# Performance work log

Measured on AMD Instinct MI355X. Metric: run time of the kernel, lower is better.

## Reference

```python
import jax, jax.numpy as jnp
import numpy as np

EPS = 1e-6
B, H, V, DH = 4096, 16, 8, 128


def setup_inputs() -> dict:
    key = jax.random.key(0)
    ks = jax.random.split(key, 7)
    s = 1.0 / np.sqrt(DH)  # ~ torch Linear init scale
    return {
        "iso_heads": jax.random.normal(ks[0], (B, H, DH), jnp.float32),
        "view_head_tokens": jax.random.normal(ks[1], (B, H, V, DH), jnp.float32),
        "pi": jax.random.uniform(ks[2], (B, H, V), jnp.float32),
        "Wq": jax.random.normal(ks[3], (H, DH, DH), jnp.float32) * s,
        "Wk": jax.random.normal(ks[4], (H, DH, DH), jnp.float32) * s,
        "Wv": jax.random.normal(ks[5], (H, DH, DH), jnp.float32) * s,
        "Wo": jax.random.normal(ks[6], (H, DH, DH), jnp.float32) * s,
    }


def reference(iso_heads, view_head_tokens, pi, Wq, Wk, Wv, Wo):
    # Per-head linears: torch Linear(y = x @ W.T), W stored (out, in) -> 'hed' (e=out, d=in)
    q = jnp.einsum("bhd,hed->bhe", iso_heads, Wq)            # [B,H,Dh]
    k = jnp.einsum("bhvd,hed->bhve", view_head_tokens, Wk)   # [B,H,V,Dh]
    v = jnp.einsum("bhvd,hed->bhve", view_head_tokens, Wv)   # [B,H,V,Dh]
    # Single-query attention per head with additive log-prior bias
    scores = jnp.einsum("bhd,bhvd->bhv", q, k) / jnp.sqrt(jnp.float32(DH))
    scores = scores + jnp.log(pi + EPS)
    attn = jax.nn.softmax(scores, axis=-1)                   # dropout = identity (eval)
    ctx = jnp.einsum("bhv,bhvd->bhd", attn, v)               # [B,H,Dh]
    out = jnp.einsum("bhd,hed->bhe", ctx, Wo)                # [B,H,Dh]
    return (out, attn)
```

## Files before the change

kernel.cpp:

```cpp
#include <hip/hip_runtime.h>
#include <cstdint>
#include <cstddef>

#define H_  16
#define V_  8
#define DH_ 128
#define B_  4096
#define BT  32
#define LDST 132

__global__ __launch_bounds__(256) void precompute_MN(
    const float* __restrict__ Wq, const float* __restrict__ Wk,
    const float* __restrict__ Wv, const float* __restrict__ Wo,
    float* __restrict__ Mmat, float* __restrict__ NTmat)
{
    const int bx    = blockIdx.x;
    const int which = bx & 1;
    const int h     = (bx >> 1) & 15;
    const int chunk = bx >> 5;
    const int tid   = threadIdx.x;
    const int col   = tid & 127;
    const int r     = chunk * 2 + (tid >> 7);

    float acc = 0.f;
    if (which == 0) {
        const float* wq = Wq + h * DH_ * DH_;
        const float* wk = Wk + h * DH_ * DH_;
#pragma unroll 8
        for (int e = 0; e < DH_; ++e)
            acc += wq[e * DH_ + r] * wk[e * DH_ + col];
        Mmat[h * DH_ * DH_ + (size_t)r * DH_ + col] = acc;
    } else {
        const float* wo = Wo + h * DH_ * DH_;
        const float* wv = Wv + h * DH_ * DH_;
#pragma unroll 8
        for (int d = 0; d < DH_; ++d)
            acc += wo[(size_t)r * DH_ + d] * wv[d * DH_ + col];
        NTmat[h * DH_ * DH_ + (size_t)col * DH_ + r] = acc;
    }
}

__global__ __launch_bounds__(256, 3) void fused_attn(
    const float* __restrict__ iso, const float* __restrict__ view,
    const float* __restrict__ pi,
    const float* __restrict__ Mmat, const float* __restrict__ NTmat,
    float* __restrict__ out, float* __restrict__ attn_out)
{
    __shared__ float wbuf[64 * DH_];
    __shared__ float row_s[BT][LDST];
    __shared__ float at_s[BT][V_];

    const int tid = threadIdx.x;
    const int h   = blockIdx.x >> 7;
    const int b0  = (blockIdx.x & 127) * BT;

    const int tx = tid & 31;
    const int ty = tid >> 5;

    const float* Mh = Mmat  + (size_t)h * DH_ * DH_;
    const float* Nh = NTmat + (size_t)h * DH_ * DH_;

#pragma unroll
    for (int i = 0; i < 4; ++i) {
        const int idx = tid + i * 256;
        const int r   = idx >> 5;
        const int q   = idx & 31;
        *(float4*)&row_s[r][q * 4] =
            *(const float4*)(iso + ((size_t)(b0 + r) * H_ + h) * DH_ + q * 4);
    }
#pragma unroll
    for (int i = 0; i < 8; ++i) {
        const int idx = tid + i * 256;
        *(float4*)&wbuf[idx * 4] = *(const float4*)(Mh + (size_t)idx * 4);
    }
    __syncthreads();

    float acc[4][4];
#pragma unroll
    for (int i = 0; i < 4; ++i)
#pragma unroll
        for (int j = 0; j < 4; ++j) acc[i][j] = 0.f;

    auto mac64 = [&](int dbase) {
#pragma unroll 4
        for (int dd = 0; dd < 64; dd += 4) {
            const float4 m0 = *(const float4*)&wbuf[(dd + 0) * DH_ + tx * 4];
            const float4 m1 = *(const float4*)&wbuf[(dd + 1) * DH_ + tx * 4];
            const float4 m2 = *(const float4*)&wbuf[(dd + 2) * DH_ + tx * 4];
            const float4 m3 = *(const float4*)&wbuf[(dd + 3) * DH_ + tx * 4];
#pragma unroll
            for (int i = 0; i < 4; ++i) {
                const float4 a = *(const float4*)&row_s[ty * 4 + i][dbase + dd];
                acc[i][0] += a.x * m0.x + a.y * m1.x + a.z * m2.x + a.w * m3.x;
                acc[i][1] += a.x * m0.y + a.y * m1.y + a.z * m2.y + a.w * m3.y;
                acc[i][2] += a.x * m0.z + a.y * m1.z + a.z * m2.z + a.w * m3.z;
                acc[i][3] += a.x * m0.w + a.y * m1.w + a.z * m2.w + a.w * m3.w;
            }
        }
    };

    mac64(0);
    __syncthreads();

#pragma unroll
    for (int i = 0; i < 8; ++i) {
        const int idx = tid + i * 256;
        *(float4*)&wbuf[idx * 4] = *(const float4*)(Mh + 8192 + (size_t)idx * 4);
    }
    __syncthreads();

    mac64(64);

#pragma unroll
    for (int i = 0; i < 4; ++i)
        *(float4*)&row_s[ty * 4 + i][tx * 4] =
            make_float4(acc[i][0], acc[i][1], acc[i][2], acc[i][3]);

    {
        const int w    = tid >> 6;
        const int lane = tid & 63;
        const int g    = lane >> 3;
        const int i8   = lane & 7;

        for (int r = 0; r < 8; ++r) {
            const int row   = w * 8 + r;
            const size_t bh = (size_t)(b0 + row) * H_ + h;
            const float* vp = view + (bh * V_ + g) * DH_ + i8 * 16;
            const float* qp = &row_s[row][i8 * 16];
            const float4 x0 = *(const float4*)(vp + 0);
            const float4 x1 = *(const float4*)(vp + 4);
            const float4 x2 = *(const float4*)(vp + 8);
            const float4 x3 = *(const float4*)(vp + 12);
            const float4 q0 = *(const float4*)(qp + 0);
            const float4 q1 = *(const float4*)(qp + 4);
            const float4 q2 = *(const float4*)(qp + 8);
            const float4 q3 = *(const float4*)(qp + 12);
            float s = x0.x*q0.x + x0.y*q0.y + x0.z*q0.z + x0.w*q0.w
                    + x1.x*q1.x + x1.y*q1.y + x1.z*q1.z + x1.w*q1.w
                    + x2.x*q2.x + x2.y*q2.y + x2.z*q2.z + x2.w*q2.w
                    + x3.x*q3.x + x3.y*q3.y + x3.z*q3.z + x3.w*q3.w;
            s += __shfl_xor(s, 1);
            s += __shfl_xor(s, 2);
            s += __shfl_xor(s, 4);
            if (i8 == 0) {
                float sc = s * 0.08838834764831845f
                         + logf(pi[bh * V_ + g] + 1e-6f);
                float mx = sc;
                mx = fmaxf(mx, __shfl_xor(mx, 8));
                mx = fmaxf(mx, __shfl_xor(mx, 16));
                mx = fmaxf(mx, __shfl_xor(mx, 32));
                const float ex = expf(sc - mx);
                float den = ex;
                den += __shfl_xor(den, 8);
                den += __shfl_xor(den, 16);
                den += __shfl_xor(den, 32);
                const float at = ex / den;
                at_s[row][g] = at;
                attn_out[bh * V_ + g] = at;
            }
        }

        const int half = lane >> 5;
        const int c    = lane & 31;
#pragma unroll
        for (int t = 0; t < 4; ++t) {
            const int row   = w * 8 + t * 2 + half;
            const size_t bh = (size_t)(b0 + row) * H_ + h;
            const float* vb = view + bh * V_ * DH_ + c * 4;
            float4 cx = make_float4(0.f, 0.f, 0.f, 0.f);
#pragma unroll
            for (int v = 0; v < V_; ++v) {
                const float a  = at_s[row][v];
                const float4 x = *(const float4*)(vb + (size_t)v * DH_);
                cx.x += a * x.x; cx.y += a * x.y; cx.z += a * x.z; cx.w += a * x.w;
            }
            *(float4*)&row_s[row][c * 4] = cx;
        }
    }
    __syncthreads();

#pragma unroll
    for (int i = 0; i < 8; ++i) {
        const int idx = tid + i * 256;
        *(float4*)&wbuf[idx * 4] = *(const float4*)(Nh + (size_t)idx * 4);
    }
    __syncthreads();

#pragma unroll
    for (int i = 0; i < 4; ++i)
#pragma unroll
        for (int j = 0; j < 4; ++j) acc[i][j] = 0.f;

    mac64(0);
    __syncthreads();

#pragma unroll
    for (int i = 0; i < 8; ++i) {
        const int idx = tid + i * 256;
        *(float4*)&wbuf[idx * 4] = *(const float4*)(Nh + 8192 + (size_t)idx * 4);
    }
    __syncthreads();

    mac64(64);

#pragma unroll
    for (int i = 0; i < 4; ++i)
        *(float4*)(out + ((size_t)(b0 + ty * 4 + i) * H_ + h) * DH_ + tx * 4) =
            make_float4(acc[i][0], acc[i][1], acc[i][2], acc[i][3]);
}

extern "C" void kernel_launch(void* const* d_in, const int* in_sizes, int n_in,
                              void* d_out, int out_size, void* d_ws, size_t ws_size,
                              hipStream_t stream)
{
    const float* iso  = (const float*)d_in[0];
    const float* view = (const float*)d_in[1];
    const float* pi   = (const float*)d_in[2];
    const float* Wq   = (const float*)d_in[3];
    const float* Wk   = (const float*)d_in[4];
    const float* Wv   = (const float*)d_in[5];
    const float* Wo   = (const float*)d_in[6];

    float* out  = (float*)d_out;
    float* attn = out + (size_t)B_ * H_ * DH_;

    float* Mmat  = (float*)d_ws;
    float* NTmat = Mmat + (size_t)H_ * DH_ * DH_;

    hipLaunchKernelGGL(precompute_MN, dim3(2048), dim3(256), 0, stream,
                       Wq, Wk, Wv, Wo, Mmat, NTmat);
    hipLaunchKernelGGL(fused_attn, dim3(H_ * (B_ / BT)), dim3(256), 0, stream,
                       iso, view, pi, Mmat, NTmat, out, attn);
}
```

Measured before the change: 484.8 us.

## Use fp16 MFMA for per-head projections and restructure attention loop

Folded weight matrices are stored as fp16 and both per-head 32x128x128 projections run on MFMA 16x16x32 f16 instructions instead of scalar FMA, with the whole weight matrix staged in shared memory at once. The view-token loop now loads each row's tokens once and reuses them for both scores and context, prefetching the next row, and replaces log(pi) plus exp with pi times exp. The N weight load overlaps with the attention stage. This cuts ALU work and global re-reads of view, at the cost of fp16 rounding of activations and weights, and occupancy drops to 2 blocks per SM.

```diff
diff --git a/kernel.cpp b/kernel.cpp
--- a/kernel.cpp
+++ b/kernel.cpp
@@ -7,12 +7,18 @@
 #define DH_ 128
 #define B_  4096
 #define BT  32
-#define LDST 132
+
+#define LDW 136
+#define LDQ 132
+
+typedef _Float16 v8h __attribute__((ext_vector_type(8)));
+typedef _Float16 v4h __attribute__((ext_vector_type(4)));
+typedef float    v4f __attribute__((ext_vector_type(4)));
 
 __global__ __launch_bounds__(256) void precompute_MN(
     const float* __restrict__ Wq, const float* __restrict__ Wk,
     const float* __restrict__ Wv, const float* __restrict__ Wo,
-    float* __restrict__ Mmat, float* __restrict__ NTmat)
+    _Float16* __restrict__ MT16, _Float16* __restrict__ N216)
 {
     const int bx    = blockIdx.x;
     const int which = bx & 1;
@@ -28,185 +34,205 @@
         const float* wk = Wk + h * DH_ * DH_;
 #pragma unroll 8
         for (int e = 0; e < DH_; ++e)
-            acc += wq[e * DH_ + r] * wk[e * DH_ + col];
-        Mmat[h * DH_ * DH_ + (size_t)r * DH_ + col] = acc;
+            acc += wq[e * DH_ + col] * wk[e * DH_ + r];
+        MT16[(size_t)h * DH_ * DH_ + r * DH_ + col] = (_Float16)acc;
     } else {
         const float* wo = Wo + h * DH_ * DH_;
         const float* wv = Wv + h * DH_ * DH_;
 #pragma unroll 8
         for (int d = 0; d < DH_; ++d)
-            acc += wo[(size_t)r * DH_ + d] * wv[d * DH_ + col];
-        NTmat[h * DH_ * DH_ + (size_t)col * DH_ + r] = acc;
+            acc += wo[r * DH_ + d] * wv[d * DH_ + col];
+        N216[(size_t)h * DH_ * DH_ + r * DH_ + col] = (_Float16)acc;
     }
 }
 
-__global__ __launch_bounds__(256, 3) void fused_attn(
+__global__ __launch_bounds__(256, 2) void fused_attn(
     const float* __restrict__ iso, const float* __restrict__ view,
     const float* __restrict__ pi,
-    const float* __restrict__ Mmat, const float* __restrict__ NTmat,
+    const _Float16* __restrict__ MT16, const _Float16* __restrict__ N216,
     float* __restrict__ out, float* __restrict__ attn_out)
 {
-    __shared__ float wbuf[64 * DH_];
-    __shared__ float row_s[BT][LDST];
-    __shared__ float at_s[BT][V_];
+    __shared__ __align__(16) _Float16 w16[128 * LDW];
+    __shared__ __align__(16) _Float16 a16[BT * LDW];
+    __shared__ __align__(16) float    qk_s[BT * LDQ];
 
     const int tid = threadIdx.x;
     const int h   = blockIdx.x >> 7;
     const int b0  = (blockIdx.x & 127) * BT;
 
-    const int tx = tid & 31;
-    const int ty = tid >> 5;
-
-    const float* Mh = Mmat  + (size_t)h * DH_ * DH_;
-    const float* Nh = NTmat + (size_t)h * DH_ * DH_;
+    const int w    = tid >> 6;
+    const int lane = tid & 63;
+    const int rt   = w >> 1;
+    const int cb   = (w & 1) * 64;
+    const int fr   = lane & 15;
+    const int kg   = lane >> 4;
 
 #pragma unroll
     for (int i = 0; i < 4; ++i) {
         const int idx = tid + i * 256;
-        const int r   = idx >> 5;
-        const int q   = idx & 31;
-        *(float4*)&row_s[r][q * 4] =
-            *(const float4*)(iso + ((size_t)(b0 + r) * H_ + h) * DH_ + q * 4);
-    }
-#pragma unroll
-    for (int i = 0; i < 8; ++i) {
-        const int idx = tid + i * 256;
-        *(float4*)&wbuf[idx * 4] = *(const float4*)(Mh + (size_t)idx * 4);
+        const int r   = idx >> 5, c4 = idx & 31;
+        const float4 t = *(const float4*)(iso + ((size_t)(b0 + r) * H_ + h) * DH_ + c4 * 4);
+        v4h ht; ht[0] = (_Float16)t.x; ht[1] = (_Float16)t.y;
+                ht[2] = (_Float16)t.z; ht[3] = (_Float16)t.w;
+        *(v4h*)&a16[r * LDW + c4 * 4] = ht;
+    }
+    {
+        const _Float16* src = MT16 + (size_t)h * DH_ * DH_;
+#pragma unroll
+        for (int i = 0; i < 8; ++i) {
+            const int idx = tid + i * 256;
+            *(v8h*)&w16[(idx >> 4) * LDW + (idx & 15) * 8] = *(const v8h*)(src + idx * 8);
+        }
     }
     __syncthreads();
 
-    float acc[4][4];
-#pragma unroll
-    for (int i = 0; i < 4; ++i)
-#pragma unroll
-        for (int j = 0; j < 4; ++j) acc[i][j] = 0.f;
-
-    auto mac64 = [&](int dbase) {
-#pragma unroll 4
-        for (int dd = 0; dd < 64; dd += 4) {
-            const float4 m0 = *(const float4*)&wbuf[(dd + 0) * DH_ + tx * 4];
-            const float4 m1 = *(const float4*)&wbuf[(dd + 1) * DH_ + tx * 4];
-            const float4 m2 = *(const float4*)&wbuf[(dd + 2) * DH_ + tx * 4];
-            const float4 m3 = *(const float4*)&wbuf[(dd + 3) * DH_ + tx * 4];
-#pragma unroll
-            for (int i = 0; i < 4; ++i) {
-                const float4 a = *(const float4*)&row_s[ty * 4 + i][dbase + dd];
-                acc[i][0] += a.x * m0.x + a.y * m1.x + a.z * m2.x + a.w * m3.x;
-                acc[i][1] += a.x * m0.y + a.y * m1.y + a.z * m2.y + a.w * m3.y;
-                acc[i][2] += a.x * m0.z + a.y * m1.z + a.z * m2.z + a.w * m3.z;
-                acc[i][3] += a.x * m0.w + a.y * m1.w + a.z * m2.w + a.w * m3.w;
-            }
-        }
-    };
-
-    mac64(0);
+    {
+        v4f ac0 = {0,0,0,0}, ac1 = {0,0,0,0}, ac2 = {0,0,0,0}, ac3 = {0,0,0,0};
+#pragma unroll
+        for (int kt = 0; kt < 4; ++kt) {
+            const int ko = kt * 32 + kg * 8;
+            const v8h a  = *(const v8h*)&a16[(rt * 16 + fr) * LDW + ko];
+            const v8h bf0 = *(const v8h*)&w16[(cb +  0 + fr) * LDW + ko];
+            const v8h bf1 = *(const v8h*)&w16[(cb + 16 + fr) * LDW + ko];
+            const v8h bf2 = *(const v8h*)&w16[(cb + 32 + fr) * LDW + ko];
+            const v8h bf3 = *(const v8h*)&w16[(cb + 48 + fr) * LDW + ko];
+            ac0 = __builtin_amdgcn_mfma_f32_16x16x32_f16(a, bf0, ac0, 0, 0, 0);
+            ac1 = __builtin_amdgcn_mfma_f32_16x16x32_f16(a, bf1, ac1, 0, 0, 0);
+            ac2 = __builtin_amdgcn_mfma_f32_16x16x32_f16(a, bf2, ac2, 0, 0, 0);
+            ac3 = __builtin_amdgcn_mfma_f32_16x16x32_f16(a, bf3, ac3, 0, 0, 0);
+        }
+#pragma unroll
+        for (int g = 0; g < 4; ++g) {
+            const int row = rt * 16 + kg * 4 + g;
+            qk_s[row * LDQ + cb +  0 + fr] = ac0[g];
+            qk_s[row * LDQ + cb + 16 + fr] = ac1[g];
+            qk_s[row * LDQ + cb + 32 + fr] = ac2[g];
+            qk_s[row * LDQ + cb + 48 + fr] = ac3[g];
+        }
+    }
     __syncthreads();
 
-#pragma unroll
-    for (int i = 0; i < 8; ++i) {
-        const int idx = tid + i * 256;
-        *(float4*)&wbuf[idx * 4] = *(const float4*)(Mh + 8192 + (size_t)idx * 4);
-    }
-    __syncthreads();
-
-    mac64(64);
-
-#pragma unroll
-    for (int i = 0; i < 4; ++i)
-        *(float4*)&row_s[ty * 4 + i][tx * 4] =
-            make_float4(acc[i][0], acc[i][1], acc[i][2], acc[i][3]);
-
-    {
-        const int w    = tid >> 6;
-        const int lane = tid & 63;
-        const int g    = lane >> 3;
-        const int i8   = lane & 7;
-
+    {
+        const _Float16* src = N216 + (size_t)h * DH_ * DH_;
+#pragma unroll
+        for (int i = 0; i < 8; ++i) {
+            const int idx = tid + i * 256;
+            *(v8h*)&w16[(idx >> 4) * LDW + (idx & 15) * 8] = *(const v8h*)(src + idx * 8);
+        }
+    }
+
+    {
+        const int hl  = lane >> 5;
+        const int l32 = lane & 31;
+        const float SC = 0.08838834764831845f;
+
+        const float* vb = view + ((size_t)(b0 + w * 8) * H_ + h) * (V_ * DH_);
+        float4 x0 = *(const float4*)(vb +   0 + lane * 4);
+        float4 x1 = *(const float4*)(vb + 256 + lane * 4);
+        float4 x2 = *(const float4*)(vb + 512 + lane * 4);
+        float4 x3 = *(const float4*)(vb + 768 + lane * 4);
+
+#pragma unroll
         for (int r = 0; r < 8; ++r) {
             const int row   = w * 8 + r;
             const size_t bh = (size_t)(b0 + row) * H_ + h;
-            const float* vp = view + (bh * V_ + g) * DH_ + i8 * 16;
-            const float* qp = &row_s[row][i8 * 16];
-            const float4 x0 = *(const float4*)(vp + 0);
-            const float4 x1 = *(const float4*)(vp + 4);
-            const float4 x2 = *(const float4*)(vp + 8);
-            const float4 x3 = *(const float4*)(vp + 12);
-            const float4 q0 = *(const float4*)(qp + 0);
-            const float4 q1 = *(const float4*)(qp + 4);
-            const float4 q2 = *(const float4*)(qp + 8);
-            const float4 q3 = *(const float4*)(qp + 12);
-            float s = x0.x*q0.x + x0.y*q0.y + x0.z*q0.z + x0.w*q0.w
-                    + x1.x*q1.x + x1.y*q1.y + x1.z*q1.z + x1.w*q1.w
-                    + x2.x*q2.x + x2.y*q2.y + x2.z*q2.z + x2.w*q2.w
-                    + x3.x*q3.x + x3.y*q3.y + x3.z*q3.z + x3.w*q3.w;
-            s += __shfl_xor(s, 1);
-            s += __shfl_xor(s, 2);
-            s += __shfl_xor(s, 4);
-            if (i8 == 0) {
-                float sc = s * 0.08838834764831845f
-                         + logf(pi[bh * V_ + g] + 1e-6f);
-                float mx = sc;
-                mx = fmaxf(mx, __shfl_xor(mx, 8));
-                mx = fmaxf(mx, __shfl_xor(mx, 16));
-                mx = fmaxf(mx, __shfl_xor(mx, 32));
-                const float ex = expf(sc - mx);
-                float den = ex;
-                den += __shfl_xor(den, 8);
-                den += __shfl_xor(den, 16);
-                den += __shfl_xor(den, 32);
-                const float at = ex / den;
-                at_s[row][g] = at;
-                attn_out[bh * V_ + g] = at;
+
+            const v4f q4 = *(const v4f*)&qk_s[row * LDQ + l32 * 4];
+            float p0 = x0.x*q4[0] + x0.y*q4[1] + x0.z*q4[2] + x0.w*q4[3];
+            float p1 = x1.x*q4[0] + x1.y*q4[1] + x1.z*q4[2] + x1.w*q4[3];
+            float p2 = x2.x*q4[0] + x2.y*q4[1] + x2.z*q4[2] + x2.w*q4[3];
+            float p3 = x3.x*q4[0] + x3.y*q4[1] + x3.z*q4[2] + x3.w*q4[3];
+
+            float4 y0, y1, y2, y3;
+            if (r < 7) {
+                const float* vn = vb + H_ * V_ * DH_;
+                y0 = *(const float4*)(vn +   0 + lane * 4);
+                y1 = *(const float4*)(vn + 256 + lane * 4);
+                y2 = *(const float4*)(vn + 512 + lane * 4);
+                y3 = *(const float4*)(vn + 768 + lane * 4);
             }
-        }
-
-        const int half = lane >> 5;
-        const int c    = lane & 31;
-#pragma unroll
-        for (int t = 0; t < 4; ++t) {
-            const int row   = w * 8 + t * 2 + half;
-            const size_t bh = (size_t)(b0 + row) * H_ + h;
-            const float* vb = view + bh * V_ * DH_ + c * 4;
-            float4 cx = make_float4(0.f, 0.f, 0.f, 0.f);
-#pragma unroll
-            for (int v = 0; v < V_; ++v) {
-                const float a  = at_s[row][v];
-                const float4 x = *(const float4*)(vb + (size_t)v * DH_);
-                cx.x += a * x.x; cx.y += a * x.y; cx.z += a * x.z; cx.w += a * x.w;
+
+            p0 += __shfl_xor(p0, 1); p0 += __shfl_xor(p0, 2); p0 += __shfl_xor(p0, 4);
+            p0 += __shfl_xor(p0, 8); p0 += __shfl_xor(p0, 16);
+            p1 += __shfl_xor(p1, 1); p1 += __shfl_xor(p1, 2); p1 += __shfl_xor(p1, 4);
+            p1 += __shfl_xor(p1, 8); p1 += __shfl_xor(p1, 16);
+            p2 += __shfl_xor(p2, 1); p2 += __shfl_xor(p2, 2); p2 += __shfl_xor(p2, 4);
+            p2 += __shfl_xor(p2, 8); p2 += __shfl_xor(p2, 16);
+            p3 += __shfl_xor(p3, 1); p3 += __shfl_xor(p3, 2); p3 += __shfl_xor(p3, 4);
+            p3 += __shfl_xor(p3, 8); p3 += __shfl_xor(p3, 16);
+            const float o0 = __shfl_xor(p0, 32);
+            const float o1 = __shfl_xor(p1, 32);
+            const float o2 = __shfl_xor(p2, 32);
+            const float o3 = __shfl_xor(p3, 32);
+
+            const float4 pa = *(const float4*)(pi + bh * V_);
+            const float4 pb = *(const float4*)(pi + bh * V_ + 4);
+            const float pe0 = hl ? pa.y : pa.x,  po0 = hl ? pa.x : pa.y;
+            const float pe1 = hl ? pa.w : pa.z,  po1 = hl ? pa.z : pa.w;
+            const float pe2 = hl ? pb.y : pb.x,  po2 = hl ? pb.x : pb.y;
+            const float pe3 = hl ? pb.w : pb.z,  po3 = hl ? pb.z : pb.w;
+
+            const float s0 = p0 * SC, s1 = p1 * SC, s2 = p2 * SC, s3 = p3 * SC;
+            const float t0 = o0 * SC, t1 = o1 * SC, t2 = o2 * SC, t3 = o3 * SC;
+            const float m  = fmaxf(fmaxf(fmaxf(s0, s1), fmaxf(s2, s3)),
+                                   fmaxf(fmaxf(t0, t1), fmaxf(t2, t3)));
+            const float e0 = (pe0 + 1e-6f) * __expf(s0 - m);
+            const float e1 = (pe1 + 1e-6f) * __expf(s1 - m);
+            const float e2 = (pe2 + 1e-6f) * __expf(s2 - m);
+            const float e3 = (pe3 + 1e-6f) * __expf(s3 - m);
+            const float f0 = (po0 + 1e-6f) * __expf(t0 - m);
+            const float f1 = (po1 + 1e-6f) * __expf(t1 - m);
+            const float f2 = (po2 + 1e-6f) * __expf(t2 - m);
+            const float f3 = (po3 + 1e-6f) * __expf(t3 - m);
+            const float inv = 1.0f / (((e0 + e1) + (e2 + e3)) + ((f0 + f1) + (f2 + f3)));
+            const float a0 = e0 * inv, a1 = e1 * inv, a2 = e2 * inv, a3 = e3 * inv;
+
+            float cx = a0 * x0.x + a1 * x1.x + a2 * x2.x + a3 * x3.x;
+            float cy = a0 * x0.y + a1 * x1.y + a2 * x2.y + a3 * x3.y;
+            float cz = a0 * x0.z + a1 * x1.z + a2 * x2.z + a3 * x3.z;
+            float cw = a0 * x0.w + a1 * x1.w + a2 * x2.w + a3 * x3.w;
+            cx += __shfl_xor(cx, 32);
+            cy += __shfl_xor(cy, 32);
+            cz += __shfl_xor(cz, 32);
+            cw += __shfl_xor(cw, 32);
+            if (lane < 32) {
+                v4h ch; ch[0] = (_Float16)cx; ch[1] = (_Float16)cy;
+                        ch[2] = (_Float16)cz; ch[3] = (_Float16)cw;
+                *(v4h*)&a16[row * LDW + l32 * 4] = ch;
             }
-            *(float4*)&row_s[row][c * 4] = cx;
+            if (l32 == 0) {
+                float* ao = attn_out + bh * V_;
+                ao[0 + hl] = a0; ao[2 + hl] = a1; ao[4 + hl] = a2; ao[6 + hl] = a3;
+            }
+            if (r < 7) { vb += H_ * V_ * DH_; x0 = y0; x1 = y1; x2 = y2; x3 = y3; }
         }
     }
     __syncthreads();
 
-#pragma unroll
-    for (int i = 0; i < 8; ++i) {
-        const int idx = tid + i * 256;
-        *(float4*)&wbuf[idx * 4] = *(const float4*)(Nh + (size_t)idx * 4);
-    }
-    __syncthreads();
-
-#pragma unroll
-    for (int i = 0; i < 4; ++i)
-#pragma unroll
-        for (int j = 0; j < 4; ++j) acc[i][j] = 0.f;
-
-    mac64(0);
-    __syncthreads();
-
-#pragma unroll
-    for (int i = 0; i < 8; ++i) {
-        const int idx = tid + i * 256;
-        *(float4*)&wbuf[idx * 4] = *(const float4*)(Nh + 8192 + (size_t)idx * 4);
-    }
-    __syncthreads();
-
-    mac64(64);
-
-#pragma unroll
-    for (int i = 0; i < 4; ++i)
-        *(float4*)(out + ((size_t)(b0 + ty * 4 + i) * H_ + h) * DH_ + tx * 4) =
-            make_float4(acc[i][0], acc[i][1], acc[i][2], acc[i][3]);
+    {
+        v4f ac0 = {0,0,0,0}, ac1 = {0,0,0,0}, ac2 = {0,0,0,0}, ac3 = {0,0,0,0};
+#pragma unroll
+        for (int kt = 0; kt < 4; ++kt) {
+            const int ko = kt * 32 + kg * 8;
+            const v8h a  = *(const v8h*)&a16[(rt * 16 + fr) * LDW + ko];
+            const v8h bf0 = *(const v8h*)&w16[(cb +  0 + fr) * LDW + ko];
+            const v8h bf1 = *(const v8h*)&w16[(cb + 16 + fr) * LDW + ko];
+            const v8h bf2 = *(const v8h*)&w16[(cb + 32 + fr) * LDW + ko];
+            const v8h bf3 = *(const v8h*)&w16[(cb + 48 + fr) * LDW + ko];
+            ac0 = __builtin_amdgcn_mfma_f32_16x16x32_f16(a, bf0, ac0, 0, 0, 0);
+            ac1 = __builtin_amdgcn_mfma_f32_16x16x32_f16(a, bf1, ac1, 0, 0, 0);
+            ac2 = __builtin_amdgcn_mfma_f32_16x16x32_f16(a, bf2, ac2, 0, 0, 0);
+            ac3 = __builtin_amdgcn_mfma_f32_16x16x32_f16(a, bf3, ac3, 0, 0, 0);
+        }
+#pragma unroll
+        for (int g = 0; g < 4; ++g) {
+            float* op = out + (size_t)(b0 + rt * 16 + kg * 4 + g) * (H_ * DH_) + h * DH_;
+            op[cb +  0 + fr] = ac0[g];
+            op[cb + 16 + fr] = ac1[g];
+            op[cb + 32 + fr] = ac2[g];
+            op[cb + 48 + fr] = ac3[g];
+        }
+    }
 }
 
 extern "C" void kernel_launch(void* const* d_in, const int* in_sizes, int n_in,
@@ -224,11 +250,11 @@
     float* out  = (float*)d_out;
     float* attn = out + (size_t)B_ * H_ * DH_;
 
-    float* Mmat  = (float*)d_ws;
-    float* NTmat = Mmat + (size_t)H_ * DH_ * DH_;
+    _Float16* MT16 = (_Float16*)d_ws;
+    _Float16* N216 = MT16 + (size_t)H_ * DH_ * DH_;
 
     hipLaunchKernelGGL(precompute_MN, dim3(2048), dim3(256), 0, stream,
-                       Wq, Wk, Wv, Wo, Mmat, NTmat);
+                       Wq, Wk, Wv, Wo, MT16, N216);
     hipLaunchKernelGGL(fused_attn, dim3(H_ * (B_ / BT)), dim3(256), 0, stream,
-                       iso, view, pi, Mmat, NTmat, out, attn);
+                       iso, view, pi, MT16, N216, out, attn);
 }
```

Result: faster. 422.1 us (-12.9%).
